# Kernel tuning notes

Hardware: AMD Instinct MI355X
Metric: run time of the kernel (lower is better)

The kernel has to match this reference:

```python
import jax, jax.numpy as jnp
import numpy as np

B, T, D, H = 64, 257, 1024, 16
F = 4096
R = 16
HD = D // H


def _layer_norm(x, g, b, eps=1e-5):
    mu = x.mean(-1, keepdims=True)
    var = x.var(-1, keepdims=True)
    return (x - mu) / jnp.sqrt(var + eps) * g + b


def _quick_gelu(x):
    return x * jax.nn.sigmoid(1.702 * x)


def _attention(x, Wq, bq, Wk, bk, Wv, bv, Wo, bo):
    scale = HD ** -0.5
    q = (x @ Wq + bq) * scale
    k = x @ Wk + bk
    v = x @ Wv + bv
    q = q.reshape(B, T, H, HD).transpose(0, 2, 1, 3)
    k = k.reshape(B, T, H, HD).transpose(0, 2, 1, 3)
    v = v.reshape(B, T, H, HD).transpose(0, 2, 1, 3)
    attn = jax.nn.softmax(jnp.einsum('bhqd,bhkd->bhqk', q, k), axis=-1)
    o = jnp.einsum('bhqk,bhkd->bhqd', attn, v)
    o = o.transpose(0, 2, 1, 3).reshape(B, T, D)
    return o @ Wo + bo


def _match_indices(metric, r, class_token=True):
    # cosine-normalized bipartite matching (no-grad path in torch; index-only here)
    m = metric / jnp.linalg.norm(metric, axis=-1, keepdims=True)
    a, b = m[:, ::2, :], m[:, 1::2, :]        # [B, ta, D], [B, tb, D]
    scores = jnp.einsum('nac,nbc->nab', a, b)  # [B, ta, tb]
    if class_token:
        scores = scores.at[:, 0, :].set(-jnp.inf)
    node_max = scores.max(-1)
    node_idx = scores.argmax(-1)
    edge_idx = jnp.argsort(-node_max, axis=-1)  # descending
    unm_idx = edge_idx[:, r:]
    src_idx = edge_idx[:, :r]
    dst_idx = jnp.take_along_axis(node_idx, src_idx, axis=-1)
    if class_token:
        unm_idx = jnp.sort(unm_idx, axis=1)
    return unm_idx, src_idx, dst_idx


def _merge_sum(x, unm_idx, src_idx, dst_idx):
    src, dst = x[:, ::2, :], x[:, 1::2, :]
    c = x.shape[-1]
    unm = jnp.take_along_axis(src, unm_idx[..., None], axis=1)       # [B, ta-r, c]
    sel = jnp.take_along_axis(src, src_idx[..., None], axis=1)       # [B, r, c]
    dst = jax.vmap(lambda d, di, sv: d.at[di].add(sv))(dst, dst_idx, sel)
    return jnp.concatenate([unm, dst], axis=1)                       # [B, T-r, c]


def setup_inputs() -> dict:
    key = jax.random.key(0)
    ks = jax.random.split(key, 12)
    s = 0.02
    return {
        'hidden_states': jax.random.normal(ks[0], (B, T, D), jnp.float32),
        'ln1_g': jnp.ones((D,), jnp.float32),
        'ln1_b': jnp.zeros((D,), jnp.float32),
        'Wq': jax.random.normal(ks[1], (D, D), jnp.float32) * s,
        'bq': jnp.zeros((D,), jnp.float32),
        'Wk': jax.random.normal(ks[2], (D, D), jnp.float32) * s,
        'bk': jnp.zeros((D,), jnp.float32),
        'Wv': jax.random.normal(ks[3], (D, D), jnp.float32) * s,
        'bv': jnp.zeros((D,), jnp.float32),
        'Wo': jax.random.normal(ks[4], (D, D), jnp.float32) * s,
        'bo': jnp.zeros((D,), jnp.float32),
        'ln2_g': jnp.ones((D,), jnp.float32),
        'ln2_b': jnp.zeros((D,), jnp.float32),
        'W1': jax.random.normal(ks[5], (D, F), jnp.float32) * s,
        'b1': jnp.zeros((F,), jnp.float32),
        'W2': jax.random.normal(ks[6], (F, D), jnp.float32) * s,
        'b2': jnp.zeros((D,), jnp.float32),
    }


def reference(hidden_states, ln1_g, ln1_b, Wq, bq, Wk, bk, Wv, bv, Wo, bo,
              ln2_g, ln2_b, W1, b1, W2, b2):
    # 1) LN1 + self-attention + residual
    x = hidden_states + _attention(_layer_norm(hidden_states, ln1_g, ln1_b),
                                   Wq, bq, Wk, bk, Wv, bv, Wo, bo)
    # 2) ToMe merge with weighted average (initial size = ones -> merge_wavg)
    metric = jax.lax.stop_gradient(x)
    unm_idx, src_idx, dst_idx = _match_indices(metric, R, class_token=True)
    size = jnp.ones((B, T, 1), x.dtype)
    x = _merge_sum(x * size, unm_idx, src_idx, dst_idx)
    size = _merge_sum(size, unm_idx, src_idx, dst_idx)
    x = x / size
    # 3) LN2 + MLP (quick_gelu) + residual
    h = _layer_norm(x, ln2_g, ln2_b)
    h = _quick_gelu(h @ W1 + b1) @ W2 + b2
    return x + h  # [B, T - R, D]
```

## Files before the change

### kernel.cpp

```cpp
#include <hip/hip_runtime.h>
#include <math.h>

#define BB 64
#define TT 257
#define DD 1024
#define HH 16
#define FF 4096
#define RR 16
#define HDD 64
#define TMM 241
#define M1 (BB*TT)
#define M2 (BB*TMM)
#define NA 129
#define NB 128

typedef float f4v __attribute__((ext_vector_type(4)));
typedef short s8v __attribute__((ext_vector_type(8)));
typedef short s4v __attribute__((ext_vector_type(4)));
typedef unsigned short us;

__device__ __forceinline__ us f2bf(float f){
  unsigned u = __float_as_uint(f);
  u += 0x7fffu + ((u >> 16) & 1u);
  return (us)(u >> 16);
}
__device__ __forceinline__ float bf2f(us h){
  return __uint_as_float(((unsigned)h) << 16);
}
__device__ __forceinline__ void splitpk(float f0, float f1, unsigned &hp, unsigned &lp){
  unsigned u0 = __float_as_uint(f0), u1 = __float_as_uint(f1);
  unsigned h0m = u0 & 0xFFFF0000u, h1m = u1 & 0xFFFF0000u;
  hp = (u0 >> 16) | h1m;
  float l0 = f0 - __uint_as_float(h0m);
  float l1 = f1 - __uint_as_float(h1m);
  lp = (__float_as_uint(l0) >> 16) | (__float_as_uint(l1) & 0xFFFF0000u);
}
__device__ __forceinline__ void gl16(const us* g, us* l){
  __builtin_amdgcn_global_load_lds((const __attribute__((address_space(1))) void*)g,
                                   (__attribute__((address_space(3))) void*)l, 16, 0, 0);
}

__global__ __launch_bounds__(64) void lnstats_kernel(const float* __restrict__ x,
                                                     float* __restrict__ st)
{
  int row = blockIdx.x, lane = threadIdx.x;
  const float* p = x + (size_t)row * DD;
  float s = 0.0f, sq = 0.0f;
  #pragma unroll
  for (int i = 0; i < 4; i++){
    float4 v = *(const float4*)(p + i * 256 + lane * 4);
    s  += v.x + v.y + v.z + v.w;
    sq += v.x*v.x + v.y*v.y + v.z*v.z + v.w*v.w;
  }
  #pragma unroll
  for (int m = 1; m < 64; m <<= 1){ s += __shfl_xor(s, m); sq += __shfl_xor(sq, m); }
  if (lane == 0){
    float mu  = s * (1.0f / DD);
    float var = sq * (1.0f / DD) - mu * mu;
    st[2*row]     = mu;
    st[2*row + 1] = 1.0f / sqrtf(var + 1e-5f);
  }
}

__global__ __launch_bounds__(256) void lncvt_kernel(const float* __restrict__ x,
    const float* __restrict__ st, const float* __restrict__ g,
    const float* __restrict__ b, us* __restrict__ out)
{
  int row = blockIdx.x, tid = threadIdx.x;
  float mu = st[2*row], rstd = st[2*row + 1];
  float4 xv = *(const float4*)(x + (size_t)row * DD + tid * 4);
  float4 gv = *(const float4*)(g + tid * 4);
  float4 bv = *(const float4*)(b + tid * 4);
  s4v o;
  o[0] = (short)f2bf((xv.x - mu) * rstd * gv.x + bv.x);
  o[1] = (short)f2bf((xv.y - mu) * rstd * gv.y + bv.y);
  o[2] = (short)f2bf((xv.z - mu) * rstd * gv.z + bv.z);
  o[3] = (short)f2bf((xv.w - mu) * rstd * gv.w + bv.w);
  *(s4v*)(out + (size_t)row * DD + tid * 4) = o;
}

__global__ __launch_bounds__(256) void wt_kernel(const float* __restrict__ src,
                                                 us* __restrict__ dhi,
                                                 us* __restrict__ dlo,
                                                 const float* __restrict__ gscale,
                                                 int K, int N)
{
  __shared__ float t[32][33];
  int tx = threadIdx.x, ty = threadIdx.y;
  int n0 = blockIdx.x * 32, k0 = blockIdx.y * 32;
  #pragma unroll
  for (int r = 0; r < 4; r++)
    t[ty + 8*r][tx] = src[(size_t)(k0 + ty + 8*r) * N + n0 + tx];
  __syncthreads();
  float gs = gscale ? gscale[k0 + tx] : 1.0f;
  #pragma unroll
  for (int r = 0; r < 4; r++){
    float f = t[tx][ty + 8*r] * gs;
    us hi = f2bf(f);
    size_t o = (size_t)(n0 + ty + 8*r) * K + k0 + tx;
    dhi[o] = hi;
    if (dlo) dlo[o] = f2bf(f - bf2f(hi));
  }
}

__global__ __launch_bounds__(256) void qc_kernel(const float* __restrict__ Wq,
    const float* __restrict__ Wk, const float* __restrict__ Wv,
    const float* __restrict__ g, const float* __restrict__ b,
    float* __restrict__ c1, float* __restrict__ c2)
{
  __shared__ float p1[4][64], p2[4][64];
  int n0 = blockIdx.x * 64;
  int kind = n0 >> 10, col0 = n0 & 1023;
  const float* W = (kind == 0) ? Wq : (kind == 1) ? Wk : Wv;
  int tx = threadIdx.x & 63, ty = threadIdx.x >> 6;
  float s1 = 0.0f, s2 = 0.0f;
  for (int k = ty; k < 1024; k += 4){
    float w = W[(size_t)k * 1024 + col0 + tx];
    s1 += g[k] * w;
    s2 += b[k] * w;
  }
  p1[ty][tx] = s1; p2[ty][tx] = s2;
  __syncthreads();
  if (ty == 0){
    c1[n0 + tx] = p1[0][tx] + p1[1][tx] + p1[2][tx] + p1[3][tx];
    c2[n0 + tx] = p2[0][tx] + p2[1][tx] + p2[2][tx] + p2[3][tx];
  }
}

__global__ __launch_bounds__(512) void qkv_kernel(const float* __restrict__ hidden,
    const us* __restrict__ WBh, const us* __restrict__ WBl,
    const float* __restrict__ bq, const float* __restrict__ bk, const float* __restrict__ bv,
    const float* __restrict__ lnstat, const float* __restrict__ c1, const float* __restrict__ c2,
    us* __restrict__ qhp, us* __restrict__ qlp, us* __restrict__ khp,
    us* __restrict__ klp, us* __restrict__ vhp, us* __restrict__ vlp)
{
  const int M = M1, K = DD;
  __shared__ __align__(16) us Ah[128*40];
  __shared__ __align__(16) us Al[128*40];
  __shared__ __align__(16) us Bh[256*32];
  __shared__ __align__(16) us Bl[256*32];
  int tid = threadIdx.x;
  int m0 = blockIdx.y * 128, n0 = blockIdx.x * 256;
  int lane = tid & 63, w = tid >> 6;
  int wr = w >> 2, wc = w & 3;
  int fr = lane & 15, fq = lane >> 4;
  f4v acc[4][4];
  f4v zero = {0.0f, 0.0f, 0.0f, 0.0f};
  #pragma unroll
  for (int i = 0; i < 4; i++)
    #pragma unroll
    for (int j = 0; j < 4; j++) acc[i][j] = zero;
  int sr = tid >> 2, sc4 = (tid & 3) * 8;
  int ar = m0 + sr; if (ar >= M) ar = M - 1;
  int lr = lane >> 2, lc = (lane & 3) * 8;
  int gb0 = n0 + w*32 + lr;

  for (int kk = 0; kk < K; kk += 32){
    {
      const float* ap = hidden + (size_t)ar * K + kk + sc4;
      float4 fa = *(const float4*)(ap);
      float4 fb = *(const float4*)(ap + 4);
      unsigned h0, h1, h2, h3, l0, l1, l2, l3;
      splitpk(fa.x, fa.y, h0, l0);
      splitpk(fa.z, fa.w, h1, l1);
      splitpk(fb.x, fb.y, h2, l2);
      splitpk(fb.z, fb.w, h3, l3);
      uint4 hv = {h0, h1, h2, h3};
      uint4 lv = {l0, l1, l2, l3};
      *(uint4*)&Ah[sr*40 + sc4] = hv;
      *(uint4*)&Al[sr*40 + sc4] = lv;
    }
    gl16(WBh + (size_t)gb0 * K + kk + lc,        &Bh[(w*32)*32]);
    gl16(WBh + (size_t)(gb0 + 16) * K + kk + lc, &Bh[(w*32 + 16)*32]);
    gl16(WBl + (size_t)gb0 * K + kk + lc,        &Bl[(w*32)*32]);
    gl16(WBl + (size_t)(gb0 + 16) * K + kk + lc, &Bl[(w*32 + 16)*32]);
    __syncthreads();
    s8v ah[4], bh[4], al[4], bl[4];
    #pragma unroll
    for (int m = 0; m < 4; m++){
      ah[m] = *(const s8v*)&Ah[(wr*64 + m*16 + fr)*40 + fq*8];
      al[m] = *(const s8v*)&Al[(wr*64 + m*16 + fr)*40 + fq*8];
    }
    #pragma unroll
    for (int n = 0; n < 4; n++){
      bh[n] = *(const s8v*)&Bh[(wc*64 + n*16 + fr)*32 + fq*8];
      bl[n] = *(const s8v*)&Bl[(wc*64 + n*16 + fr)*32 + fq*8];
    }
    #pragma unroll
    for (int m = 0; m < 4; m++)
      #pragma unroll
      for (int n = 0; n < 4; n++){
        acc[m][n] = __builtin_amdgcn_mfma_f32_16x16x32_bf16(ah[m], bh[n], acc[m][n], 0, 0, 0);
        acc[m][n] = __builtin_amdgcn_mfma_f32_16x16x32_bf16(ah[m], bl[n], acc[m][n], 0, 0, 0);
        acc[m][n] = __builtin_amdgcn_mfma_f32_16x16x32_bf16(al[m], bh[n], acc[m][n], 0, 0, 0);
      }
    __syncthreads();
  }
  int kind = n0 >> 10;
  const float* bsel = (kind == 0) ? bq : (kind == 1) ? bk : bv;
  us* O0 = (kind == 0) ? qhp : (kind == 1) ? khp : vhp;
  us* O1 = (kind == 0) ? qlp : (kind == 1) ? klp : vlp;
  float scl = (kind == 0) ? 0.125f : 1.0f;
  float C1r[4], C2r[4];
  int h2r[4], d2r[4];
  #pragma unroll
  for (int n = 0; n < 4; n++){
    int gcol = n0 + wc*64 + n*16 + fr;
    int lcn = gcol & 1023;
    h2r[n] = lcn >> 6; d2r[n] = lcn & 63;
    C1r[n] = c1[gcol];
    C2r[n] = c2[gcol] + bsel[lcn];
  }
  #pragma unroll
  for (int m = 0; m < 4; m++){
    int grow0 = m0 + wr*64 + m*16 + fq*4;
    #pragma unroll
    for (int i = 0; i < 4; i++){
      int grow = grow0 + i;
      if (grow < M){
        float mu = lnstat[2*grow], rstd = lnstat[2*grow + 1];
        int b2 = grow / 257, t2 = grow - b2 * 257;
        size_t rb = ((size_t)(b2*16) * 257 + t2) * 64;
        #pragma unroll
        for (int n = 0; n < 4; n++){
          size_t off2 = rb + (size_t)h2r[n] * (257*64) + d2r[n];
          float v = (rstd * acc[m][n][i] - rstd * mu * C1r[n] + C2r[n]) * scl;
          us hi = f2bf(v);
          O0[off2] = hi;
          O1[off2] = f2bf(v - bf2f(hi));
        }
      }
    }
  }
}

template<int AMODE, int SPLIT, int EPI>
__global__ __launch_bounds__(256) void gemm2_kernel(const us* __restrict__ Ahp,
    const us* __restrict__ Alp,
    const us* __restrict__ BTh, const us* __restrict__ BTl,
    const float* __restrict__ bias, const float* __restrict__ resid,
    void* __restrict__ C0, int M, int N, int K)
{
  __shared__ __align__(16) us Ah[128*32];
  __shared__ __align__(16) us Bh[128*32];
  __shared__ __align__(16) us Al[SPLIT ? 128*32 : 8];
  __shared__ __align__(16) us Bl[SPLIT ? 128*32 : 8];
  int tid = threadIdx.x;
  int m0 = blockIdx.y * 128, n0 = blockIdx.x * 128;
  int lane = tid & 63, w = tid >> 6;
  int wr = w >> 1, wc = w & 1;
  int fr = lane & 15, fq = lane >> 4;
  f4v acc[4][4];
  f4v zero = {0.0f, 0.0f, 0.0f, 0.0f};
  #pragma unroll
  for (int i = 0; i < 4; i++)
    #pragma unroll
    for (int j = 0; j < 4; j++) acc[i][j] = zero;
  int lr = lane >> 2, lc = (lane & 3) * 8;
  int ga0 = m0 + w*32 + lr;      if (ga0 >= M) ga0 = M - 1;
  int ga1 = m0 + w*32 + 16 + lr; if (ga1 >= M) ga1 = M - 1;
  int gb0 = n0 + w*32 + lr;
  int b2a = ga0 / 257, t2a = ga0 - b2a * 257;
  int b2b = ga1 / 257, t2b = ga1 - b2b * 257;

  for (int kk = 0; kk < K; kk += 32){
    if (AMODE == 1){
      gl16(Ahp + (size_t)ga0 * K + kk + lc, &Ah[(w*32)*32]);
      gl16(Ahp + (size_t)ga1 * K + kk + lc, &Ah[(w*32 + 16)*32]);
      if (SPLIT){
        gl16(Alp + (size_t)ga0 * K + kk + lc, &Al[(w*32)*32]);
        gl16(Alp + (size_t)ga1 * K + kk + lc, &Al[(w*32 + 16)*32]);
      }
    } else {
      int h2 = kk >> 6, d2 = (kk & 63) + lc;
      size_t o0 = ((size_t)(b2a*16 + h2) * 257 + t2a) * 64 + d2;
      size_t o1 = ((size_t)(b2b*16 + h2) * 257 + t2b) * 64 + d2;
      gl16(Ahp + o0, &Ah[(w*32)*32]);
      gl16(Ahp + o1, &Ah[(w*32 + 16)*32]);
      if (SPLIT){
        gl16(Alp + o0, &Al[(w*32)*32]);
        gl16(Alp + o1, &Al[(w*32 + 16)*32]);
      }
    }
    gl16(BTh + (size_t)gb0 * K + kk + lc,        &Bh[(w*32)*32]);
    gl16(BTh + (size_t)(gb0 + 16) * K + kk + lc, &Bh[(w*32 + 16)*32]);
    if (SPLIT){
      gl16(BTl + (size_t)gb0 * K + kk + lc,        &Bl[(w*32)*32]);
      gl16(BTl + (size_t)(gb0 + 16) * K + kk + lc, &Bl[(w*32 + 16)*32]);
    }
    __syncthreads();
    s8v ah[4], bh[4], al[4], bl[4];
    #pragma unroll
    for (int m = 0; m < 4; m++){
      ah[m] = *(const s8v*)&Ah[(wr*64 + m*16 + fr)*32 + fq*8];
      if (SPLIT) al[m] = *(const s8v*)&Al[(wr*64 + m*16 + fr)*32 + fq*8];
    }
    #pragma unroll
    for (int n = 0; n < 4; n++){
      bh[n] = *(const s8v*)&Bh[(wc*64 + n*16 + fr)*32 + fq*8];
      if (SPLIT) bl[n] = *(const s8v*)&Bl[(wc*64 + n*16 + fr)*32 + fq*8];
    }
    #pragma unroll
    for (int m = 0; m < 4; m++)
      #pragma unroll
      for (int n = 0; n < 4; n++){
        acc[m][n] = __builtin_amdgcn_mfma_f32_16x16x32_bf16(ah[m], bh[n], acc[m][n], 0, 0, 0);
        if (SPLIT){
          acc[m][n] = __builtin_amdgcn_mfma_f32_16x16x32_bf16(ah[m], bl[n], acc[m][n], 0, 0, 0);
          acc[m][n] = __builtin_amdgcn_mfma_f32_16x16x32_bf16(al[m], bh[n], acc[m][n], 0, 0, 0);
        }
      }
    __syncthreads();
  }
  #pragma unroll
  for (int m = 0; m < 4; m++){
    int grow0 = m0 + wr*64 + m*16 + fq*4;
    #pragma unroll
    for (int n = 0; n < 4; n++){
      int gcol = n0 + wc*64 + n*16 + fr;
      float bcol = bias[gcol];
      #pragma unroll
      for (int i = 0; i < 4; i++){
        int grow = grow0 + i;
        if (grow < M){
          float v = acc[m][n][i] + bcol;
          size_t off = (size_t)grow * N + gcol;
          if (EPI == 1){
            ((float*)C0)[off] = v + resid[off];
          } else {
            float gq = v / (1.0f + expf(-1.702f * v));
            ((us*)C0)[off] = f2bf(gq);
          }
        }
      }
    }
  }
}

__global__ __launch_bounds__(512, 1) void attn_flash_kernel(
    const us* __restrict__ Qh, const us* __restrict__ Ql,
    const us* __restrict__ Kh, const us* __restrict__ Klo,
    const us* __restrict__ Vh, const us* __restrict__ Vlo,
    us* Oh, us* Ol)
{
  __shared__ __align__(16) us Kl[257 * 128];
  __shared__ __align__(16) us Vl[64 * 640];
  int bh = blockIdx.x;
  const size_t hb = (size_t)bh * 257 * 64;
  int tid = threadIdx.x;
  int l = tid & 63, w = tid >> 6;
  int g = l >> 4, c = l & 15;
  const float NEG = -3.0e38f;

  {
    s8v z8 = {0,0,0,0,0,0,0,0};
    for (int idx = tid; idx < 64*640/8; idx += 512)
      *((s8v*)Vl + idx) = z8;
  }
  __syncthreads();
  for (int idx = tid; idx < 257*8; idx += 512){
    int tok = idx >> 3, ch = idx & 7;
    int sw = (tok & 7) << 4;
    s8v hv = *(const s8v*)(Kh  + hb + (size_t)tok * 64 + ch*8);
    s8v lv = *(const s8v*)(Klo + hb + (size_t)tok * 64 + ch*8);
    char* kr = (char*)Kl + tok * 256;
    *(s8v*)(kr + ((ch*16) ^ sw)) = hv;
    *(s8v*)(kr + 128 + ((ch*16) ^ sw)) = lv;
  }
  for (int idx = tid; idx < 257*8; idx += 512){
    int tok = idx >> 3, ch = idx & 7;
    s8v hv = *(const s8v*)(Vh  + hb + (size_t)tok * 64 + ch*8);
    s8v lv = *(const s8v*)(Vlo + hb + (size_t)tok * 64 + ch*8);
    #pragma unroll
    for (int j = 0; j < 8; j++){
      int d = ch*8 + j;
      char* vr = (char*)Vl + d * 1280;
      int off = (tok * 2) ^ (j << 4);
      *(us*)(vr + off) = (us)hv[j];
      *(us*)(vr + 640 + off) = (us)lv[j];
    }
  }
  __syncthreads();

  for (int qt = w; qt < 17; qt += 8){
    int t0 = qt * 16;
    int qr = t0 + c; if (qr > 256) qr = 256;
    const us* qp  = Qh + hb + (size_t)qr * 64 + g*8;
    const us* qp2 = Ql + hb + (size_t)qr * 64 + g*8;
    s8v qhi[2], qlo[2];
    qhi[0] = *(const s8v*)(qp);       qhi[1] = *(const s8v*)(qp + 32);
    qlo[0] = *(const s8v*)(qp2);      qlo[1] = *(const s8v*)(qp2 + 32);

    float m_run = NEG, l_run = 0.0f;
    f4v o4[4];
    #pragma unroll
    for (int dt = 0; dt < 4; dt++) o4[dt] = (f4v){0.0f, 0.0f, 0.0f, 0.0f};

    #pragma unroll 1
    for (int mck = 0; mck < 9; mck++){
      f4v a0, a1;
      {
        int t = 2*mck;
        int krow = t * 16 + c; if (krow > 256) krow = 256;
        char* kr = (char*)Kl + krow * 256;
        int sw = (krow & 7) << 4;
        s8v khi0 = *(const s8v*)(kr + ((g * 16) ^ sw));
        s8v khi1 = *(const s8v*)(kr + ((64 + g * 16) ^ sw));
        s8v klo0 = *(const s8v*)(kr + 128 + ((g * 16) ^ sw));
        s8v klo1 = *(const s8v*)(kr + 128 + ((64 + g * 16) ^ sw));
        f4v a = {0.0f, 0.0f, 0.0f, 0.0f};
        a = __builtin_amdgcn_mfma_f32_16x16x32_bf16(khi0, qhi[0], a, 0, 0, 0);
        a = __builtin_amdgcn_mfma_f32_16x16x32_bf16(khi1, qhi[1], a, 0, 0, 0);
        a = __builtin_amdgcn_mfma_f32_16x16x32_bf16(khi0, qlo[0], a, 0, 0, 0);
        a = __builtin_amdgcn_mfma_f32_16x16x32_bf16(khi1, qlo[1], a, 0, 0, 0);
        a = __builtin_amdgcn_mfma_f32_16x16x32_bf16(klo0, qhi[0], a, 0, 0, 0);
        a = __builtin_amdgcn_mfma_f32_16x16x32_bf16(klo1, qhi[1], a, 0, 0, 0);
        a0 = a;
      }
      if (mck < 8){
        int t = 2*mck + 1;
        int krow = t * 16 + c; if (krow > 256) krow = 256;
        char* kr = (char*)Kl + krow * 256;
        int sw = (krow & 7) << 4;
        s8v khi0 = *(const s8v*)(kr + ((g * 16) ^ sw));
        s8v khi1 = *(const s8v*)(kr + ((64 + g * 16) ^ sw));
        s8v klo0 = *(const s8v*)(kr + 128 + ((g * 16) ^ sw));
        s8v klo1 = *(const s8v*)(kr + 128 + ((64 + g * 16) ^ sw));
        f4v a = {0.0f, 0.0f, 0.0f, 0.0f};
        a = __builtin_amdgcn_mfma_f32_16x16x32_bf16(khi0, qhi[0], a, 0, 0, 0);
        a = __builtin_amdgcn_mfma_f32_16x16x32_bf16(khi1, qhi[1], a, 0, 0, 0);
        a = __builtin_amdgcn_mfma_f32_16x16x32_bf16(khi0, qlo[0], a, 0, 0, 0);
        a = __builtin_amdgcn_mfma_f32_16x16x32_bf16(khi1, qlo[1], a, 0, 0, 0);
        a = __builtin_amdgcn_mfma_f32_16x16x32_bf16(klo0, qhi[0], a, 0, 0, 0);
        a = __builtin_amdgcn_mfma_f32_16x16x32_bf16(klo1, qhi[1], a, 0, 0, 0);
        a1 = a;
      } else {
        a1 = (f4v){NEG, NEG, NEG, NEG};
        a0[0] = (g == 0) ? a0[0] : NEG;
        a0[1] = NEG; a0[2] = NEG; a0[3] = NEG;
      }
      float cm = fmaxf(fmaxf(fmaxf(a0[0], a0[1]), fmaxf(a0[2], a0[3])),
                       fmaxf(fmaxf(a1[0], a1[1]), fmaxf(a1[2], a1[3])));
      cm = fmaxf(cm, __shfl_xor(cm, 16));
      cm = fmaxf(cm, __shfl_xor(cm, 32));
      float m_new = fmaxf(m_run, cm);
      float scl = __expf(m_run - m_new);
      m_run = m_new;
      l_run *= scl;
      #pragma unroll
      for (int dt = 0; dt < 4; dt++){
        o4[dt][0] *= scl; o4[dt][1] *= scl; o4[dt][2] *= scl; o4[dt][3] *= scl;
      }
      float ls = 0.0f;
      unsigned Ph2[2][2], Pl2[2][2];
      #pragma unroll
      for (int k2 = 0; k2 < 2; k2++){
        float e0 = __expf(a0[2*k2] - m_new), e1 = __expf(a0[2*k2+1] - m_new);
        ls += e0 + e1;
        us h0 = f2bf(e0), h1 = f2bf(e1);
        Ph2[0][k2] = (unsigned)h0 | ((unsigned)h1 << 16);
        Pl2[0][k2] = (unsigned)f2bf(e0 - bf2f(h0)) | ((unsigned)f2bf(e1 - bf2f(h1)) << 16);
        float e2 = __expf(a1[2*k2] - m_new), e3 = __expf(a1[2*k2+1] - m_new);
        ls += e2 + e3;
        us h2 = f2bf(e2), h3 = f2bf(e3);
        Ph2[1][k2] = (unsigned)h2 | ((unsigned)h3 << 16);
        Pl2[1][k2] = (unsigned)f2bf(e2 - bf2f(h2)) | ((unsigned)f2bf(e3 - bf2f(h3)) << 16);
      }
      l_run += ls;
      s8v pbh, pbl;
      #pragma unroll
      for (int ww = 0; ww < 4; ww++){
        int srcl = (((g & 1) * 2 + (ww >> 1)) << 4) | c;
        unsigned h0 = (unsigned)__shfl((int)Ph2[0][ww & 1], srcl, 64);
        unsigned lo0 = (unsigned)__shfl((int)Pl2[0][ww & 1], srcl, 64);
        unsigned h1 = (unsigned)__shfl((int)Ph2[1][ww & 1], srcl, 64);
        unsigned lo1 = (unsigned)__shfl((int)Pl2[1][ww & 1], srcl, 64);
        ((unsigned*)&pbh)[ww] = (g >> 1) ? h1 : h0;
        ((unsigned*)&pbl)[ww] = (g >> 1) ? lo1 : lo0;
      }
      #pragma unroll
      for (int dt = 0; dt < 4; dt++){
        int d = dt * 16 + c;
        char* vr = (char*)Vl + d * 1280;
        int off = (mck * 64 + g * 16) ^ ((d & 7) << 4);
        s8v vh = *(const s8v*)(vr + off);
        s8v vlo = *(const s8v*)(vr + 640 + off);
        o4[dt] = __builtin_amdgcn_mfma_f32_16x16x32_bf16(vh, pbh, o4[dt], 0, 0, 0);
        o4[dt] = __builtin_amdgcn_mfma_f32_16x16x32_bf16(vh, pbl, o4[dt], 0, 0, 0);
        o4[dt] = __builtin_amdgcn_mfma_f32_16x16x32_bf16(vlo, pbh, o4[dt], 0, 0, 0);
      }
    }
    l_run += __shfl_xor(l_run, 16);
    l_run += __shfl_xor(l_run, 32);
    float inv = 1.0f / l_run;
    int qrow = t0 + c;
    if (qrow <= 256){
      us* oph = Oh + hb + (size_t)qrow * 64;
      us* opl = Ol + hb + (size_t)qrow * 64;
      #pragma unroll
      for (int dt = 0; dt < 4; dt++){
        s4v hv4, lv4;
        #pragma unroll
        for (int i = 0; i < 4; i++){
          float ov = o4[dt][i] * inv;
          us hi = f2bf(ov);
          hv4[i] = (short)hi;
          lv4[i] = (short)f2bf(ov - bf2f(hi));
        }
        *(s4v*)(oph + dt*16 + g*4) = hv4;
        *(s4v*)(opl + dt*16 + g*4) = lv4;
      }
    }
  }
}

__global__ __launch_bounds__(64) void norms_kernel(const float* __restrict__ x, float* __restrict__ nrm)
{
  int row = blockIdx.x, lane = threadIdx.x;
  const float* p = x + (size_t)row * DD;
  float sq = 0.0f;
  #pragma unroll
  for (int i = 0; i < 4; i++){
    float4 v = *(const float4*)(p + i * 256 + lane * 4);
    sq += v.x*v.x + v.y*v.y + v.z*v.z + v.w*v.w;
  }
  #pragma unroll
  for (int m = 1; m < 64; m <<= 1) sq += __shfl_xor(sq, m);
  if (lane == 0) nrm[row] = sqrtf(sq);
}

__global__ __launch_bounds__(256) void scores_kernel(const float* __restrict__ x,
                                                     const float* __restrict__ nrm,
                                                     float* __restrict__ sc)
{
  __shared__ __align__(16) float as_[16][1028];
  __shared__ __align__(16) float bs_[16][1028];
  int it = blockIdx.x, b = blockIdx.y;
  int tid = threadIdx.x;
  int rloc = tid >> 4, chunk = tid & 15;
  {
    int i = it * 16 + rloc;
    int tg = (i < NA) ? 2 * i : 2 * (NA - 1);
    const float* p = x + ((size_t)b * TT + tg) * DD + chunk * 64;
    #pragma unroll
    for (int ii = 0; ii < 16; ii++)
      *(float4*)&as_[rloc][chunk * 64 + 4*ii] = *(const float4*)(p + 4*ii);
  }
  for (int jt = 0; jt < 8; jt++){
    __syncthreads();
    {
      int j = jt * 16 + rloc;
      const float* p = x + ((size_t)b * TT + 2*j + 1) * DD + chunk * 64;
      #pragma unroll
      for (int ii = 0; ii < 16; ii++)
        *(float4*)&bs_[rloc][chunk * 64 + 4*ii] = *(const float4*)(p + 4*ii);
    }
    __syncthreads();
    int iloc = tid >> 4, jloc = tid & 15;
    float sum = 0.0f;
    #pragma unroll 8
    for (int cgg = 0; cgg < 1024; cgg += 4){
      float4 av = *(const float4*)&as_[iloc][cgg];
      float4 bvv = *(const float4*)&bs_[jloc][cgg];
      sum += av.x*bvv.x + av.y*bvv.y + av.z*bvv.z + av.w*bvv.w;
    }
    int i = it * 16 + iloc, j = jt * 16 + jloc;
    if (i < NA){
      float val = sum / (nrm[(size_t)b * TT + 2*i] * nrm[(size_t)b * TT + 2*j + 1]);
      sc[((size_t)b * NA + i) * NB + j] = val;
    }
  }
}

__global__ __launch_bounds__(64) void node_kernel(const float* __restrict__ sc,
                                                  float* __restrict__ nmax, int* __restrict__ nidx)
{
  int i = blockIdx.x, b = blockIdx.y, lane = threadIdx.x;
  const float* row = sc + ((size_t)b * NA + i) * NB;
  float v0 = row[lane];
  float v1 = row[lane + 64];
  float bv = v0; int bi = lane;
  if (v1 > bv){ bv = v1; bi = lane + 64; }
  #pragma unroll
  for (int m = 1; m < 64; m <<= 1){
    float ov = __shfl_xor(bv, m);
    int oi = __shfl_xor(bi, m);
    if (ov > bv || (ov == bv && oi < bi)){ bv = ov; bi = oi; }
  }
  if (lane == 0){
    if (i == 0){ nmax[(size_t)b * NA] = -INFINITY; nidx[(size_t)b * NA] = 0; }
    else { nmax[(size_t)b * NA + i] = bv; nidx[(size_t)b * NA + i] = bi; }
  }
}

__global__ __launch_bounds__(256) void rank_kernel(const float* __restrict__ nmax,
    const int* __restrict__ nidx, int* __restrict__ src, int* __restrict__ dst,
    int* __restrict__ unm, int* __restrict__ cnt)
{
  __shared__ float v[NA];
  __shared__ int rk[NA];
  __shared__ int edge[NA];
  __shared__ int cs[NB];
  int b = blockIdx.x, t = threadIdx.x;
  if (t < NA) v[t] = nmax[(size_t)b * NA + t];
  if (t < NB) cs[t] = 0;
  __syncthreads();
  if (t < NA){
    float vt = v[t]; int r = 0;
    for (int i = 0; i < NA; i++){
      float vi = v[i];
      r += (vi > vt) || (vi == vt && i < t);
    }
    rk[t] = r; edge[r] = t;
  }
  __syncthreads();
  if (t < RR){
    int s = edge[t];
    src[b * RR + t] = s;
    int d = nidx[(size_t)b * NA + s];
    dst[b * RR + t] = d;
    atomicAdd(&cs[d], 1);
  }
  if (t < NA && rk[t] >= RR){
    int p = 0;
    for (int i = 0; i < NA; i++) p += (i < t) && (rk[i] >= RR);
    unm[b * (NA - RR) + p] = t;
  }
  __syncthreads();
  if (t < NB) cnt[b * NB + t] = cs[t];
}

__global__ __launch_bounds__(256) void merge_kernel(const float* __restrict__ x,
    const int* __restrict__ src, const int* __restrict__ dst, const int* __restrict__ unm,
    const int* __restrict__ cnt, float* __restrict__ xm)
{
  int u = blockIdx.x, b = blockIdx.y;
  int c = threadIdx.x * 4;
  const float* xb = x + (size_t)b * TT * DD;
  float4 acc;
  if (u < NA - RR){
    int ts = 2 * unm[b * (NA - RR) + u];
    acc = *(const float4*)(xb + (size_t)ts * DD + c);
  } else {
    int j = u - (NA - RR);
    acc = *(const float4*)(xb + (size_t)(2*j + 1) * DD + c);
    #pragma unroll
    for (int k2 = 0; k2 < RR; k2++){
      if (dst[b * RR + k2] == j){
        int ts = 2 * src[b * RR + k2];
        float4 av = *(const float4*)(xb + (size_t)ts * DD + c);
        acc.x += av.x; acc.y += av.y; acc.z += av.z; acc.w += av.w;
      }
    }
    float inv = 1.0f / (float)(1 + cnt[b * NB + j]);
    acc.x *= inv; acc.y *= inv; acc.z *= inv; acc.w *= inv;
  }
  *(float4*)(xm + ((size_t)b * TMM + u) * DD + c) = acc;
}

extern "C" void kernel_launch(void* const* d_in, const int* in_sizes, int n_in,
                              void* d_out, int out_size, void* d_ws, size_t ws_size,
                              hipStream_t stream)
{
  (void)in_sizes; (void)n_in; (void)out_size; (void)ws_size;
  const float* hidden = (const float*)d_in[0];
  const float* ln1_g  = (const float*)d_in[1];
  const float* ln1_b  = (const float*)d_in[2];
  const float* Wq = (const float*)d_in[3];
  const float* bq = (const float*)d_in[4];
  const float* Wk = (const float*)d_in[5];
  const float* bk = (const float*)d_in[6];
  const float* Wv = (const float*)d_in[7];
  const float* bv = (const float*)d_in[8];
  const float* Wo = (const float*)d_in[9];
  const float* bo = (const float*)d_in[10];
  const float* ln2_g = (const float*)d_in[11];
  const float* ln2_b = (const float*)d_in[12];
  const float* W1 = (const float*)d_in[13];
  const float* b1 = (const float*)d_in[14];
  const float* W2 = (const float*)d_in[15];
  const float* b2 = (const float*)d_in[16];

  char* base = (char*)d_ws;
  const size_t PE = (size_t)M1 * DD;
  const size_t PL = PE * sizeof(us);
  us* qh = (us*)base;          us* ql = qh + PE;
  us* kh = (us*)(base + 2*PL); us* kl = kh + PE;
  us* vh = (us*)(base + 4*PL); us* vl = vh + PE;
  us* wts = (us*)(base + 6*PL);
  const size_t WD = (size_t)DD * DD;
  us* wqh = wts;
  us* wkh = wqh + WD;
  us* wvh = wkh + WD;
  us* wql = wvh + WD;
  us* wkl = wql + WD;
  us* wvl = wkl + WD;
  us* woh = wvl + WD;
  us* wol = woh + WD;
  us* w1h = wol + WD;
  us* w2h = w1h + (size_t)DD * FF;
  float* lnst1 = (float*)(w2h + (size_t)FF * DD);
  float* c1p   = lnst1 + 2 * M1;
  float* c2p   = c1p + 3072;
  float* xb = (float*)(base + 2*PL);
  float* nrm   = (float*)(base + 4*PL);
  float* sc    = nrm + M1;
  float* nmaxp = sc + (size_t)BB * NA * NB;
  int*   nidxp = (int*)(nmaxp + BB * NA);
  int*   srcI  = nidxp + BB * NA;
  int*   dstI  = srcI + BB * RR;
  int*   unmI  = dstI + BB * RR;
  int*   cntI  = unmI + BB * (NA - RR);
  us*    xh2   = (us*)(base + 4*PL + (size_t)8*1024*1024);
  float* lnst2 = (float*)(base + 4*PL + (size_t)48*1024*1024);
  float* xm = (float*)d_out;
  us* mid = (us*)base;

  dim3 tb32(32, 8);
  wt_kernel<<<dim3(DD/32, DD/32), tb32, 0, stream>>>(Wq, wqh, wql, ln1_g, DD, DD);
  wt_kernel<<<dim3(DD/32, DD/32), tb32, 0, stream>>>(Wk, wkh, wkl, ln1_g, DD, DD);
  wt_kernel<<<dim3(DD/32, DD/32), tb32, 0, stream>>>(Wv, wvh, wvl, ln1_g, DD, DD);
  wt_kernel<<<dim3(DD/32, DD/32), tb32, 0, stream>>>(Wo, woh, wol, nullptr, DD, DD);
  wt_kernel<<<dim3(FF/32, DD/32), tb32, 0, stream>>>(W1, w1h, nullptr, nullptr, DD, FF);
  wt_kernel<<<dim3(DD/32, FF/32), tb32, 0, stream>>>(W2, w2h, nullptr, nullptr, FF, DD);

  qc_kernel<<<48, 256, 0, stream>>>(Wq, Wk, Wv, ln1_g, ln1_b, c1p, c2p);
  lnstats_kernel<<<M1, 64, 0, stream>>>(hidden, lnst1);

  qkv_kernel<<<dim3(3072/256, (M1 + 127)/128), 512, 0, stream>>>(hidden, wqh, wql,
      bq, bk, bv, lnst1, c1p, c2p, qh, ql, kh, kl, vh, vl);

  attn_flash_kernel<<<BB*HH, 512, 0, stream>>>(qh, ql, kh, kl, vh, vl, qh, ql);

  gemm2_kernel<2,1,1><<<dim3(DD/128, (M1 + 127)/128), 256, 0, stream>>>(qh, ql, woh, wol,
      bo, hidden, xb, M1, DD, DD);

  norms_kernel<<<M1, 64, 0, stream>>>(xb, nrm);
  scores_kernel<<<dim3(9, BB), 256, 0, stream>>>(xb, nrm, sc);
  node_kernel<<<dim3(NA, BB), 64, 0, stream>>>(sc, nmaxp, nidxp);
  rank_kernel<<<BB, 256, 0, stream>>>(nmaxp, nidxp, srcI, dstI, unmI, cntI);
  merge_kernel<<<dim3(TMM, BB), 256, 0, stream>>>(xb, srcI, dstI, unmI, cntI, xm);

  lnstats_kernel<<<M2, 64, 0, stream>>>(xm, lnst2);
  lncvt_kernel<<<M2, 256, 0, stream>>>(xm, lnst2, ln2_g, ln2_b, xh2);

  gemm2_kernel<1,0,2><<<dim3(FF/128, (M2 + 127)/128), 256, 0, stream>>>(xh2, nullptr, w1h, nullptr,
      b1, nullptr, mid, M2, FF, DD);
  gemm2_kernel<1,0,1><<<dim3(DD/128, (M2 + 127)/128), 256, 0, stream>>>(mid, nullptr, w2h, nullptr,
      b2, xm, (float*)d_out, M2, DD, FF);
}
```

Before: 1.584 ms.

## Use 256x256 triple-buffered 8-wave bf16 GEMM for the MLP layers

Adds a new GEMM kernel with 256x256 output tiles, 512 threads (8 waves), a three-stage LDS ring with asynchronous global-to-LDS loads, and prefetch split across two half-tile MFMA phases with priority boosting. The two MLP GEMMs (W1 with quick_gelu epilogue, W2 with residual epilogue) switch from the 128x128 single-precision-split kernel to this one. The larger tiles raise arithmetic intensity and reduce global traffic per FLOP. The cost is fewer blocks (wave quantization on M2=15424 rows), higher register and LDS pressure, and partial waste in the last row tile.

```diff
diff --git a/kernel.cpp b/kernel.cpp
--- a/kernel.cpp
+++ b/kernel.cpp
@@ -335,6 +335,136 @@
       }
     }
   }
+}
+
+template<int EPI>
+__global__ __launch_bounds__(512) void gemm8p_kernel(const us* __restrict__ A,
+    const us* __restrict__ B, const float* __restrict__ bias,
+    const float* __restrict__ resid, void* __restrict__ C, int M, int N, int K)
+{
+  __shared__ __align__(16) us As[3][256*32];
+  __shared__ __align__(16) us Bs[3][256*32];
+  int tid = threadIdx.x;
+  int m0 = blockIdx.y * 256, n0 = blockIdx.x * 256;
+  int lane = tid & 63, w = tid >> 6;
+  int wr = w >> 2, wc = w & 3;
+  int fr = lane & 15, fq = lane >> 4;
+  f4v acc[8][4];
+  f4v zero = {0.0f, 0.0f, 0.0f, 0.0f};
+  #pragma unroll
+  for (int i = 0; i < 8; i++)
+    #pragma unroll
+    for (int j = 0; j < 4; j++) acc[i][j] = zero;
+  int srow = w*16 + (lane >> 2);
+  int aR0 = m0 + srow;        if (aR0 >= M) aR0 = M - 1;
+  int aR1 = m0 + 128 + srow;  if (aR1 >= M) aR1 = M - 1;
+  int bR0 = n0 + srow;
+  int bR1 = n0 + 128 + srow;
+  int o16 = ((lane & 3) * 8) ^ (((srow >> 3) & 1) << 4);
+  int ldst = w * 512;
+
+  const int NT = K >> 5;
+  #pragma unroll
+  for (int t0 = 0; t0 < 2; t0++){
+    gl16(A + (size_t)aR0 * K + t0*32 + o16, &As[t0][ldst]);
+    gl16(B + (size_t)bR0 * K + t0*32 + o16, &Bs[t0][ldst]);
+    gl16(A + (size_t)aR1 * K + t0*32 + o16, &As[t0][4096 + ldst]);
+    gl16(B + (size_t)bR1 * K + t0*32 + o16, &Bs[t0][4096 + ldst]);
+  }
+  asm volatile("s_waitcnt vmcnt(4)" ::: "memory");
+  __builtin_amdgcn_s_barrier();
+
+  int buf = 0;
+  #pragma unroll 1
+  for (int t = 0; t < NT; ++t){
+    int nbuf = buf + 2; if (nbuf >= 3) nbuf -= 3;
+    bool pf = (t + 2) < NT;
+    int kk2 = (t + 2) * 32;
+    us* Ab = As[buf];
+    us* Bb = Bs[buf];
+    {
+      s8v a[4], b[4];
+      #pragma unroll
+      for (int mt = 0; mt < 4; mt++){
+        int r = wr*128 + mt*16 + fr;
+        a[mt] = *(const s8v*)&Ab[r*32 + (fq*8 ^ (((r >> 3) & 1) << 4))];
+      }
+      #pragma unroll
+      for (int nt = 0; nt < 4; nt++){
+        int r = wc*64 + nt*16 + fr;
+        b[nt] = *(const s8v*)&Bb[r*32 + (fq*8 ^ (((r >> 3) & 1) << 4))];
+      }
+      if (pf){
+        gl16(A + (size_t)aR0 * K + kk2 + o16, &As[nbuf][ldst]);
+        gl16(B + (size_t)bR0 * K + kk2 + o16, &Bs[nbuf][ldst]);
+      }
+      __builtin_amdgcn_s_barrier();
+      __builtin_amdgcn_s_setprio(1);
+      #pragma unroll
+      for (int mt = 0; mt < 4; mt++)
+        #pragma unroll
+        for (int nt = 0; nt < 4; nt++)
+          acc[mt][nt] = __builtin_amdgcn_mfma_f32_16x16x32_bf16(a[mt], b[nt], acc[mt][nt], 0, 0, 0);
+      __builtin_amdgcn_s_setprio(0);
+      __builtin_amdgcn_s_barrier();
+    }
+    {
+      s8v a[4], b[4];
+      #pragma unroll
+      for (int mt = 0; mt < 4; mt++){
+        int r = wr*128 + 64 + mt*16 + fr;
+        a[mt] = *(const s8v*)&Ab[r*32 + (fq*8 ^ (((r >> 3) & 1) << 4))];
+      }
+      #pragma unroll
+      for (int nt = 0; nt < 4; nt++){
+        int r = wc*64 + nt*16 + fr;
+        b[nt] = *(const s8v*)&Bb[r*32 + (fq*8 ^ (((r >> 3) & 1) << 4))];
+      }
+      if (pf){
+        gl16(A + (size_t)aR1 * K + kk2 + o16, &As[nbuf][4096 + ldst]);
+        gl16(B + (size_t)bR1 * K + kk2 + o16, &Bs[nbuf][4096 + ldst]);
+      }
+      __builtin_amdgcn_s_barrier();
+      __builtin_amdgcn_s_setprio(1);
+      #pragma unroll
+      for (int mt = 0; mt < 4; mt++)
+        #pragma unroll
+        for (int nt = 0; nt < 4; nt++)
+          acc[4 + mt][nt] = __builtin_amdgcn_mfma_f32_16x16x32_bf16(a[mt], b[nt], acc[4 + mt][nt], 0, 0, 0);
+      __builtin_amdgcn_s_setprio(0);
+    }
+    if (t + 1 < NT){
+      if (pf) asm volatile("s_waitcnt vmcnt(4)" ::: "memory");
+      else    asm volatile("s_waitcnt vmcnt(0)" ::: "memory");
+    }
+    __builtin_amdgcn_s_barrier();
+    buf = buf + 1; if (buf >= 3) buf = 0;
+  }
+  #pragma unroll
+  for (int mh = 0; mh < 2; mh++)
+    #pragma unroll
+    for (int mt = 0; mt < 4; mt++){
+      int grow0 = m0 + wr*128 + mh*64 + mt*16 + fq*4;
+      #pragma unroll
+      for (int nt = 0; nt < 4; nt++){
+        int gcol = n0 + wc*64 + nt*16 + fr;
+        float bcol = bias[gcol];
+        #pragma unroll
+        for (int i = 0; i < 4; i++){
+          int grow = grow0 + i;
+          if (grow < M){
+            float v = acc[mh*4 + mt][nt][i] + bcol;
+            size_t off = (size_t)grow * N + gcol;
+            if (EPI == 1){
+              ((float*)C)[off] = v + resid[off];
+            } else {
+              float gq = v / (1.0f + expf(-1.702f * v));
+              ((us*)C)[off] = f2bf(gq);
+            }
+          }
+        }
+      }
+    }
 }
 
 __global__ __launch_bounds__(512, 1) void attn_flash_kernel(
@@ -744,8 +874,8 @@
   lnstats_kernel<<<M2, 64, 0, stream>>>(xm, lnst2);
   lncvt_kernel<<<M2, 256, 0, stream>>>(xm, lnst2, ln2_g, ln2_b, xh2);
 
-  gemm2_kernel<1,0,2><<<dim3(FF/128, (M2 + 127)/128), 256, 0, stream>>>(xh2, nullptr, w1h, nullptr,
+  gemm8p_kernel<2><<<dim3(FF/256, (M2 + 255)/256), 512, 0, stream>>>(xh2, w1h,
       b1, nullptr, mid, M2, FF, DD);
-  gemm2_kernel<1,0,1><<<dim3(DD/128, (M2 + 127)/128), 256, 0, stream>>>(mid, nullptr, w2h, nullptr,
+  gemm8p_kernel<1><<<dim3(DD/256, (M2 + 255)/256), 512, 0, stream>>>(mid, w2h,
       b2, xm, (float*)d_out, M2, DD, FF);
 }
```

Result: faster. 1.548 ms (-2.3%).
